# Performance work log

Hardware: AMD Instinct MI355X
Metric: run time of the kernel (lower is better)

## Reference

```python
import jax, jax.numpy as jnp
import numpy as np

HIDDEN = 3072
HEADS = 32
HEAD_DIM = HIDDEN // HEADS  # 96


def setup_inputs() -> dict:
    key = jax.random.key(0)
    k1, k2, k3, k4 = jax.random.split(key, 4)
    B, S = 2, 2048
    x = jax.random.normal(k1, (B, S, HIDDEN), dtype=jnp.float32)
    # qkv_proj: Linear(hidden, 3*hidden, bias=False); torch weight is [out,in]
    w_qkv = jax.random.normal(k2, (3 * HIDDEN, HIDDEN), dtype=jnp.float32) * (HIDDEN ** -0.5)
    # o_proj: Linear(hidden, hidden) with bias
    w_o = jax.random.normal(k3, (HIDDEN, HIDDEN), dtype=jnp.float32) * (HIDDEN ** -0.5)
    b_o = jax.random.normal(k4, (HIDDEN,), dtype=jnp.float32) * 0.01
    return {"x": x, "w_qkv": w_qkv, "w_o": w_o, "b_o": b_o}


def reference(x, w_qkv, w_o, b_o):
    B, S, _ = x.shape
    qkv = jnp.einsum('bsh,oh->bso', x, w_qkv)  # [B,S,3*HIDDEN]
    q, k, v = jnp.split(qkv, 3, axis=-1)
    # [B,S,HIDDEN] -> [B,H,S,D]
    def split_heads(t):
        return t.reshape(B, S, HEADS, HEAD_DIM).transpose(0, 2, 1, 3)
    q, k, v = split_heads(q), split_heads(k), split_heads(v)
    scores = jnp.einsum('bhqd,bhkd->bhqk', q, k) / jnp.sqrt(jnp.float32(HEAD_DIM))
    attn = jax.nn.softmax(scores, axis=-1)
    out = jnp.einsum('bhqk,bhkd->bhqd', attn, v)  # [B,H,S,D]
    out = out.transpose(0, 2, 1, 3).reshape(B, S, HIDDEN)
    return jnp.einsum('bsh,oh->bso', out, w_o) + b_o
```

## Files before the change

### kernel.cpp

```cpp
#include <hip/hip_runtime.h>
#include <math.h>


typedef unsigned int u32;
typedef unsigned short u16;
typedef __attribute__((ext_vector_type(8))) short bf16x8;
typedef __attribute__((ext_vector_type(4))) float f32x4;
typedef __attribute__((ext_vector_type(16))) float f32x16;

#define MFMA(a, b, c) __builtin_amdgcn_mfma_f32_16x16x32_bf16((a), (b), (c), 0, 0, 0)
#define MFMA32(a, b, c) __builtin_amdgcn_mfma_f32_32x32x16_bf16((a), (b), (c), 0, 0, 0)

#define GLDS16(g, l) __builtin_amdgcn_global_load_lds( \
    (const __attribute__((address_space(1))) u32*)(g), \
    (__attribute__((address_space(3))) u32*)(l), 16, 0, 0)

__device__ __forceinline__ u16 f2bf(float f) {
  u32 u = __builtin_bit_cast(u32, f);
  return (u16)((u + 0x7fffu + ((u >> 16) & 1u)) >> 16);
}
__device__ __forceinline__ float bf2f(u16 h) {
  u32 u = ((u32)h) << 16;
  return __builtin_bit_cast(float, u);
}
__device__ __forceinline__ void split2(float f, u16& h, u16& l) {
  h = f2bf(f);
  l = f2bf(f - bf2f(h));
}
__device__ __forceinline__ bf16x8 ld16(const u16* p) {
  return *reinterpret_cast<const bf16x8*>(p);
}

__global__ void split_kernel(const float* __restrict__ src, u16* __restrict__ dst,
                             long n) {
  long i = ((long)blockIdx.x * 256 + threadIdx.x) * 4;
  if (i >= n) return;
  const float4 v = *reinterpret_cast<const float4*>(src + i);
  const u32 i32 = (u32)i;
  const u32 row = i32 / 3072u;
  const u32 col = i32 - row * 3072u;
  const long base = (long)row * 6144 + (col >> 5) * 64 + (col & 31);
  ushort4 h, l;
  split2(v.x, h.x, l.x);
  split2(v.y, h.y, l.y);
  split2(v.z, h.z, l.z);
  split2(v.w, h.w, l.w);
  *reinterpret_cast<ushort4*>(dst + base) = h;
  *reinterpret_cast<ushort4*>(dst + base + 32) = l;
}

template <int MODE>
__global__ __launch_bounds__(256, 2) void gemm32(
    const u16* __restrict__ A2, const u16* __restrict__ B2,
    int M, int N,
    u16* __restrict__ C2, float* __restrict__ Cf, const float* __restrict__ bias) {
  constexpr int NT = 96;
  __shared__ u16 ldsA[2][128 * 64];
  __shared__ u16 ldsB[2][192 * 64];
  const int tid = threadIdx.x;
  const int lane = tid & 63;
  const int w = tid >> 6;
  const int wm = w >> 1, wn = w & 1;
  const int l31 = lane & 31;
  const int l5 = lane >> 5;

  const int mt = M >> 7;
  const int nwg = gridDim.x;
  const int bid = blockIdx.x;
  const int wg = (bid & 7) * (nwg >> 3) + (bid >> 3);
  const int bm = wg % mt, bn = wg / mt;

  const int srow = lane >> 3;
  const int sgc = ((lane & 7) ^ srow ^ w) * 8;

  auto stA = [&](int buf, int kt, int j) {
    const int r = j * 32 + w * 8 + srow;
    GLDS16(A2 + (long)(bm * 128 + r) * 6144 + kt * 64 + sgc,
           &ldsA[buf][(j * 32 + w * 8) * 64]);
  };
  auto stB = [&](int buf, int kt, int j) {
    const int r = j * 32 + w * 8 + srow;
    GLDS16(B2 + (long)(bn * 192 + r) * 6144 + kt * 64 + sgc,
           &ldsB[buf][(j * 32 + w * 8) * 64]);
  };

  f32x16 acc[2][3];
#pragma unroll
  for (int m = 0; m < 2; ++m)
#pragma unroll
    for (int n = 0; n < 3; ++n)
#pragma unroll
      for (int j = 0; j < 16; ++j) acc[m][n][j] = 0.f;

  stA(0, 0, 0); stA(0, 0, 1); stA(0, 0, 2); stA(0, 0, 3);
  stB(0, 0, 0); stB(0, 0, 1); stB(0, 0, 2);
  stB(0, 0, 3); stB(0, 0, 4); stB(0, 0, 5);
  __syncthreads();

  const int aRow0 = wm * 64 + l31;
  const int bRow0 = wn * 96 + l31;
  const int rk = (lane & 7) ^ ((lane >> 3) & 3);

#define CSLOT(KS, PL) ((((KS)*2 + l5 + (PL)*4) ^ rk) * 8)
#define RD_PH(KS)                                                          \
  _Pragma("unroll") for (int n = 0; n < 3; ++n) {                          \
    const int off = (bRow0 + n * 32) * 64;                                 \
    b[n][0] = ld16(&LB[off + CSLOT(KS, 0)]);                               \
    b[n][1] = ld16(&LB[off + CSLOT(KS, 1)]);                               \
  }                                                                        \
  _Pragma("unroll") for (int m = 0; m < 2; ++m) {                          \
    const int off = (aRow0 + m * 32) * 64;                                 \
    a[m][0] = ld16(&LA[off + CSLOT(KS, 0)]);                               \
    a[m][1] = ld16(&LA[off + CSLOT(KS, 1)]);                               \
  }
#define DO_MFMA3()                                                         \
  __builtin_amdgcn_s_setprio(1);                                           \
  _Pragma("unroll") for (int m = 0; m < 2; ++m)                            \
  _Pragma("unroll") for (int n = 0; n < 3; ++n) {                          \
    acc[m][n] = MFMA32(a[m][0], b[n][0], acc[m][n]);                       \
    acc[m][n] = MFMA32(a[m][0], b[n][1], acc[m][n]);                       \
    acc[m][n] = MFMA32(a[m][1], b[n][0], acc[m][n]);                       \
  }                                                                        \
  __builtin_amdgcn_s_setprio(0);
#define PH_SYNC()                                                          \
  __builtin_amdgcn_s_barrier();                                            \
  asm volatile("s_waitcnt lgkmcnt(0)" ::: "memory");                       \
  __builtin_amdgcn_sched_barrier(0);

  for (int t = 0; t < NT; ++t) {
    const int cur = t & 1;
    const int nxt = cur ^ 1;
    const u16* LA = ldsA[cur];
    const u16* LB = ldsB[cur];
    bf16x8 a[2][2], b[3][2];
    RD_PH(0);
    if (t + 1 < NT) {
      stA(nxt, t + 1, 0); stA(nxt, t + 1, 1);
      stA(nxt, t + 1, 2); stA(nxt, t + 1, 3);
      stB(nxt, t + 1, 0); stB(nxt, t + 1, 1); stB(nxt, t + 1, 2);
      stB(nxt, t + 1, 3); stB(nxt, t + 1, 4); stB(nxt, t + 1, 5);
    }
    PH_SYNC();
    DO_MFMA3();
    __builtin_amdgcn_s_barrier();
    RD_PH(1);
    PH_SYNC();
    DO_MFMA3();
    asm volatile("s_waitcnt vmcnt(0)" ::: "memory");
    __builtin_amdgcn_s_barrier();
  }
#undef CSLOT
#undef RD_PH
#undef DO_MFMA3
#undef PH_SYNC

#pragma unroll
  for (int mf = 0; mf < 2; ++mf)
#pragma unroll
    for (int nf = 0; nf < 3; ++nf) {
      const int col = bn * 192 + wn * 96 + nf * 32 + l31;
#pragma unroll
      for (int reg = 0; reg < 16; ++reg) {
        const int rif = (reg & 3) + 8 * (reg >> 2) + 4 * l5;
        const long row = (long)bm * 128 + wm * 64 + mf * 32 + rif;
        const float v = acc[mf][nf][reg];
        if (MODE == 0) {
          const long idx = row * (2L * N) + (col >> 5) * 64 + (col & 31);
          u16 h, l;
          split2(v, h, l);
          C2[idx] = h;
          C2[idx + 32] = l;
        } else {
          Cf[row * N + col] = v + bias[col];
        }
      }
    }
}

__global__ void pack_k(const u16* __restrict__ QKV2, u16* __restrict__ Kp) {
  const int t = blockIdx.x * 256 + threadIdx.x;
  const int lane = t & 63;
  const int rec3 = t >> 6;
  const int c = rec3 % 3;
  const int kb = (rec3 / 3) & 127;
  const int hl = rec3 / 384;
  const int lr = lane & 15, lg = lane >> 4;
  const long src = ((long)((hl >> 5) * 2048 + kb * 16 + lr)) * 18432 +
                   (96 + (hl & 31) * 3 + c) * 64 + lg * 8;
  const long dst = ((long)rec3 * 2) * 512 + lane * 8;
  *reinterpret_cast<bf16x8*>(Kp + dst) = ld16(QKV2 + src);
  *reinterpret_cast<bf16x8*>(Kp + dst + 512) = ld16(QKV2 + src + 32);
}

__global__ __launch_bounds__(256) void pack_v(const u16* __restrict__ QKV2,
                                              u16* __restrict__ Vp) {
  __shared__ u16 sV[2][32 * 96];
  const int tid = threadIdx.x;
  const int hl = blockIdx.x >> 6;
  const int kq = blockIdx.x & 63;
  const long rowbase = ((long)((hl >> 5) * 2048 + kq * 32)) * 18432 +
                       (192 + (hl & 31) * 3) * 64;
#pragma unroll
  for (int i = 0; i < 3; ++i) {
    const int idx = i * 256 + tid;
    const int pl = idx / 384;
    const int r2 = idx % 384;
    const int row = r2 / 12, cu = r2 % 12;
    const long src = rowbase + (long)row * 18432 + (cu >> 2) * 64 + (cu & 3) * 8 + pl * 32;
    *reinterpret_cast<bf16x8*>(&sV[pl][row * 96 + cu * 8]) = ld16(QKV2 + src);
  }
  __syncthreads();
#pragma unroll
  for (int i = 0; i < 3; ++i) {
    const int idx = i * 256 + tid;
    const int lane = idx & 63;
    const int rl = idx >> 6;
    const int n = rl >> 1, pl = rl & 1;
    const int lr = lane & 15, lg = lane >> 4;
    bf16x8 o;
#pragma unroll
    for (int e = 0; e < 8; ++e) o[e] = (short)sV[pl][(lg * 8 + e) * 96 + n * 16 + lr];
    const long dst = ((((long)hl * 6 + n) * 64 + kq) * 2 + pl) * 512 + lane * 8;
    *reinterpret_cast<bf16x8*>(Vp + dst) = o;
  }
}

__global__ __launch_bounds__(256, 2) void attn_kernel(
    const u16* __restrict__ QKV2,
    const u16* __restrict__ Kp, const u16* __restrict__ Vp,
    u16* __restrict__ AO2) {
  __shared__ u16 kv[2][24 * 512];
  __shared__ u16 pb[4][2][512];
  const int lane = threadIdx.x & 63;
  const int wv = threadIdx.x >> 6;
  const int lr = lane & 15, lg = lane >> 4;

  const int nwg = gridDim.x;
  const int bid = blockIdx.x;
  const int wg = (bid & 7) * (nwg >> 3) + (bid >> 3);
  const int hl = wg >> 5;
  const int qblk = wg & 31;
  const int b = hl >> 5;
  const int q0 = qblk * 64 + wv * 16;

  bf16x8 qh[3], ql[3];
  {
    const long qofs =
        ((long)(b * 2048 + q0 + lr)) * 18432 + ((hl & 31) * 3) * 64 + lg * 8;
#pragma unroll
    for (int c = 0; c < 3; ++c) {
      qh[c] = ld16(QKV2 + qofs + c * 64);
      ql[c] = ld16(QKV2 + qofs + c * 64 + 32);
    }
  }

  f32x4 o_acc[6];
#pragma unroll
  for (int n = 0; n < 6; ++n)
#pragma unroll
    for (int j = 0; j < 4; ++j) o_acc[n][j] = 0.f;
  float lsum[4] = {0.f, 0.f, 0.f, 0.f};

  const float scale = 0.10206207261596577f;
  u16* pbh = pb[wv][0];
  u16* pbl = pb[wv][1];

  auto stage = [&](int nb, int it) {
    const long kbase = ((long)hl * 768 + (long)it * 12) * 512;
    const long vbase = ((long)hl * 768 + (long)it * 2) * 512;
#pragma unroll
    for (int j = 0; j < 6; ++j) {
      const int r = wv * 6 + j;
      const u16* src;
      if (r < 12) {
        const int tt = r / 6, rc = r % 6;
        src = Kp + kbase + ((long)(tt * 6 + rc)) * 512 + lane * 8;
      } else {
        const int r2 = r - 12;
        src = Vp + vbase + ((long)((r2 >> 1) * 128 + (r2 & 1))) * 512 + lane * 8;
      }
      GLDS16(src, &kv[nb][r * 512]);
    }
  };

  stage(0, 0);
  __syncthreads();

  for (int it = 0; it < 64; ++it) {
    const int nb = it & 1;
    if (it < 63) stage(nb ^ 1, it + 1);
    const u16* L = kv[nb];

    f32x4 s0, s1;
#pragma unroll
    for (int j = 0; j < 4; ++j) { s0[j] = 0.f; s1[j] = 0.f; }
#pragma unroll
    for (int c = 0; c < 3; ++c) {
      const bf16x8 kh0 = ld16(L + (c * 2 + 0) * 512 + lane * 8);
      const bf16x8 kl0 = ld16(L + (c * 2 + 1) * 512 + lane * 8);
      const bf16x8 kh1 = ld16(L + (6 + c * 2 + 0) * 512 + lane * 8);
      const bf16x8 kl1 = ld16(L + (6 + c * 2 + 1) * 512 + lane * 8);
      s0 = MFMA(qh[c], kh0, s0);
      s1 = MFMA(qh[c], kh1, s1);
      s0 = MFMA(qh[c], kl0, s0);
      s1 = MFMA(qh[c], kl1, s1);
      s0 = MFMA(ql[c], kh0, s0);
      s1 = MFMA(ql[c], kh1, s1);
    }

#pragma unroll
    for (int j = 0; j < 4; ++j) {
      const float p0 = __expf(fmaf(s0[j], scale, -12.f));
      const float p1 = __expf(fmaf(s1[j], scale, -12.f));
      lsum[j] += p0 + p1;
      const int r = lg * 4 + j;
      const int key = j ^ lg;
      u16 h, l;
      split2(p0, h, l);
      const int a0 = r * 32 + ((((lr >> 3) ^ key) & 3) << 3) + (lr & 7);
      pbh[a0] = h;
      pbl[a0] = l;
      split2(p1, h, l);
      const int a1 = r * 32 + ((((2 + (lr >> 3)) ^ key) & 3) << 3) + (lr & 7);
      pbh[a1] = h;
      pbl[a1] = l;
    }
    const int rkey = (lr & 3) ^ (lr >> 2);
    const int ra = lr * 32 + (((lg ^ rkey) & 3) << 3);
    const bf16x8 pah = ld16(&pbh[ra]);
    const bf16x8 pal = ld16(&pbl[ra]);

#pragma unroll
    for (int n = 0; n < 6; ++n) {
      const bf16x8 vh = ld16(L + (12 + n * 2 + 0) * 512 + lane * 8);
      const bf16x8 vl = ld16(L + (12 + n * 2 + 1) * 512 + lane * 8);
      o_acc[n] = MFMA(pah, vh, o_acc[n]);
      o_acc[n] = MFMA(pah, vl, o_acc[n]);
      o_acc[n] = MFMA(pal, vh, o_acc[n]);
    }
    __syncthreads();
  }

  float inv[4];
#pragma unroll
  for (int j = 0; j < 4; ++j) {
    float rs = lsum[j];
#pragma unroll
    for (int mk = 1; mk < 16; mk <<= 1) rs += __shfl_xor(rs, mk);
    inv[j] = 1.f / rs;
  }
#pragma unroll
  for (int n = 0; n < 6; ++n)
#pragma unroll
    for (int j = 0; j < 4; ++j) {
      const long row = (long)(b * 2048 + q0 + lg * 4 + j);
      const long idx =
          row * 6144 + ((hl & 31) * 3 + (n >> 1)) * 64 + (n & 1) * 16 + lr;
      u16 h, l;
      split2(o_acc[n][j] * inv[j], h, l);
      AO2[idx] = h;
      AO2[idx + 32] = l;
    }
}

extern "C" void kernel_launch(void* const* d_in, const int* in_sizes, int n_in,
                              void* d_out, int out_size, void* d_ws, size_t ws_size,
                              hipStream_t stream) {
  const float* x = (const float*)d_in[0];
  const float* wqkv = (const float*)d_in[1];
  const float* wo = (const float*)d_in[2];
  const float* bo = (const float*)d_in[3];
  float* out = (float*)d_out;
  char* ws = (char*)d_ws;

  const size_t E_X = (size_t)4096 * 3072;
  const size_t E_WQ = (size_t)9216 * 3072;
  const size_t E_QKV = (size_t)4096 * 9216;
  const size_t E_WO = (size_t)3072 * 3072;

  u16* X2 = (u16*)ws;
  char* W0 = ws + 4 * E_X;
  u16* W2 = (u16*)W0;
  char* Q0 = W0 + 4 * E_WQ;
  u16* QKV2 = (u16*)Q0;
  char* V0 = Q0 + 4 * E_QKV;
  u16* VP = (u16*)V0;
  u16* KP = (u16*)ws;
  u16* AO2 = (u16*)W0;
  u16* WO2 = (u16*)(W0 + 4 * E_X);

  const size_t need = 4 * (E_X + E_WQ + E_QKV + E_X);
  if (ws_size < need) return;

  split_kernel<<<12288, 256, 0, stream>>>(x, X2, (long)E_X);
  split_kernel<<<27648, 256, 0, stream>>>(wqkv, W2, (long)E_WQ);
  gemm32<0><<<1536, 256, 0, stream>>>(X2, W2, 4096, 9216, QKV2, nullptr, nullptr);
  pack_k<<<6144, 256, 0, stream>>>(QKV2, KP);
  pack_v<<<4096, 256, 0, stream>>>(QKV2, VP);
  split_kernel<<<9216, 256, 0, stream>>>(wo, WO2, (long)E_WO);
  attn_kernel<<<2048, 256, 0, stream>>>(QKV2, KP, VP, AO2);
  gemm32<1><<<512, 256, 0, stream>>>(AO2, WO2, 4096, 3072, nullptr, out, bo);
}
```

Baseline: 1.318 ms.

## Process two 16-row query fragments per wave to reuse staged K/V tiles

Each wave now handles 32 query rows (two fragments) instead of 16, so each workgroup covers 128 queries and the grid is halved. The K and V values loaded from LDS, and the K/V tiles staged from global memory, are reused across both fragments, cutting LDS reads and global K/V traffic per query. In exchange, registers roughly double for accumulators and Q fragments, which may hurt occupancy under the two-blocks-per-CU launch bound. The grid of 1024 workgroups is also coarser across the CUs.

```diff
diff --git a/kernel.cpp b/kernel.cpp
--- a/kernel.cpp
+++ b/kernel.cpp
@@ -230,7 +230,7 @@
     const u16* __restrict__ Kp, const u16* __restrict__ Vp,
     u16* __restrict__ AO2) {
   __shared__ u16 kv[2][24 * 512];
-  __shared__ u16 pb[4][2][512];
+  __shared__ u16 pb[4][2][2][512];
   const int lane = threadIdx.x & 63;
   const int wv = threadIdx.x >> 6;
   const int lr = lane & 15, lg = lane >> 4;
@@ -238,32 +238,33 @@
   const int nwg = gridDim.x;
   const int bid = blockIdx.x;
   const int wg = (bid & 7) * (nwg >> 3) + (bid >> 3);
-  const int hl = wg >> 5;
-  const int qblk = wg & 31;
+  const int hl = wg >> 4;
+  const int qblk = wg & 15;
   const int b = hl >> 5;
-  const int q0 = qblk * 64 + wv * 16;
-
-  bf16x8 qh[3], ql[3];
-  {
+  const int q0 = qblk * 128 + wv * 32;
+
+  bf16x8 qh[2][3], ql[2][3];
+#pragma unroll
+  for (int f = 0; f < 2; ++f) {
     const long qofs =
-        ((long)(b * 2048 + q0 + lr)) * 18432 + ((hl & 31) * 3) * 64 + lg * 8;
+        ((long)(b * 2048 + q0 + f * 16 + lr)) * 18432 + ((hl & 31) * 3) * 64 + lg * 8;
 #pragma unroll
     for (int c = 0; c < 3; ++c) {
-      qh[c] = ld16(QKV2 + qofs + c * 64);
-      ql[c] = ld16(QKV2 + qofs + c * 64 + 32);
-    }
-  }
-
-  f32x4 o_acc[6];
-#pragma unroll
-  for (int n = 0; n < 6; ++n)
-#pragma unroll
-    for (int j = 0; j < 4; ++j) o_acc[n][j] = 0.f;
-  float lsum[4] = {0.f, 0.f, 0.f, 0.f};
+      qh[f][c] = ld16(QKV2 + qofs + c * 64);
+      ql[f][c] = ld16(QKV2 + qofs + c * 64 + 32);
+    }
+  }
+
+  f32x4 o_acc[2][6];
+#pragma unroll
+  for (int f = 0; f < 2; ++f)
+#pragma unroll
+    for (int n = 0; n < 6; ++n)
+#pragma unroll
+      for (int j = 0; j < 4; ++j) o_acc[f][n][j] = 0.f;
+  float lsum[2][4] = {{0.f, 0.f, 0.f, 0.f}, {0.f, 0.f, 0.f, 0.f}};
 
   const float scale = 0.10206207261596577f;
-  u16* pbh = pb[wv][0];
-  u16* pbl = pb[wv][1];
 
   auto stage = [&](int nb, int it) {
     const long kbase = ((long)hl * 768 + (long)it * 12) * 512;
@@ -291,76 +292,92 @@
     if (it < 63) stage(nb ^ 1, it + 1);
     const u16* L = kv[nb];
 
-    f32x4 s0, s1;
-#pragma unroll
-    for (int j = 0; j < 4; ++j) { s0[j] = 0.f; s1[j] = 0.f; }
+    bf16x8 kh0[3], kl0[3], kh1[3], kl1[3];
 #pragma unroll
     for (int c = 0; c < 3; ++c) {
-      const bf16x8 kh0 = ld16(L + (c * 2 + 0) * 512 + lane * 8);
-      const bf16x8 kl0 = ld16(L + (c * 2 + 1) * 512 + lane * 8);
-      const bf16x8 kh1 = ld16(L + (6 + c * 2 + 0) * 512 + lane * 8);
-      const bf16x8 kl1 = ld16(L + (6 + c * 2 + 1) * 512 + lane * 8);
-      s0 = MFMA(qh[c], kh0, s0);
-      s1 = MFMA(qh[c], kh1, s1);
-      s0 = MFMA(qh[c], kl0, s0);
-      s1 = MFMA(qh[c], kl1, s1);
-      s0 = MFMA(ql[c], kh0, s0);
-      s1 = MFMA(ql[c], kh1, s1);
-    }
-
-#pragma unroll
-    for (int j = 0; j < 4; ++j) {
-      const float p0 = __expf(fmaf(s0[j], scale, -12.f));
-      const float p1 = __expf(fmaf(s1[j], scale, -12.f));
-      lsum[j] += p0 + p1;
-      const int r = lg * 4 + j;
-      const int key = j ^ lg;
-      u16 h, l;
-      split2(p0, h, l);
-      const int a0 = r * 32 + ((((lr >> 3) ^ key) & 3) << 3) + (lr & 7);
-      pbh[a0] = h;
-      pbl[a0] = l;
-      split2(p1, h, l);
-      const int a1 = r * 32 + ((((2 + (lr >> 3)) ^ key) & 3) << 3) + (lr & 7);
-      pbh[a1] = h;
-      pbl[a1] = l;
-    }
-    const int rkey = (lr & 3) ^ (lr >> 2);
-    const int ra = lr * 32 + (((lg ^ rkey) & 3) << 3);
-    const bf16x8 pah = ld16(&pbh[ra]);
-    const bf16x8 pal = ld16(&pbl[ra]);
+      kh0[c] = ld16(L + (c * 2 + 0) * 512 + lane * 8);
+      kl0[c] = ld16(L + (c * 2 + 1) * 512 + lane * 8);
+      kh1[c] = ld16(L + (6 + c * 2 + 0) * 512 + lane * 8);
+      kl1[c] = ld16(L + (6 + c * 2 + 1) * 512 + lane * 8);
+    }
+
+    bf16x8 pah[2], pal[2];
+#pragma unroll
+    for (int f = 0; f < 2; ++f) {
+      f32x4 s0, s1;
+#pragma unroll
+      for (int j = 0; j < 4; ++j) { s0[j] = 0.f; s1[j] = 0.f; }
+#pragma unroll
+      for (int c = 0; c < 3; ++c) {
+        s0 = MFMA(qh[f][c], kh0[c], s0);
+        s1 = MFMA(qh[f][c], kh1[c], s1);
+        s0 = MFMA(qh[f][c], kl0[c], s0);
+        s1 = MFMA(qh[f][c], kl1[c], s1);
+        s0 = MFMA(ql[f][c], kh0[c], s0);
+        s1 = MFMA(ql[f][c], kh1[c], s1);
+      }
+      u16* pbh = pb[wv][f][0];
+      u16* pbl = pb[wv][f][1];
+#pragma unroll
+      for (int j = 0; j < 4; ++j) {
+        const float p0 = __expf(fmaf(s0[j], scale, -12.f));
+        const float p1 = __expf(fmaf(s1[j], scale, -12.f));
+        lsum[f][j] += p0 + p1;
+        const int r = lg * 4 + j;
+        const int key = j ^ lg;
+        u16 h, l;
+        split2(p0, h, l);
+        const int a0 = r * 32 + ((((lr >> 3) ^ key) & 3) << 3) + (lr & 7);
+        pbh[a0] = h;
+        pbl[a0] = l;
+        split2(p1, h, l);
+        const int a1 = r * 32 + ((((2 + (lr >> 3)) ^ key) & 3) << 3) + (lr & 7);
+        pbh[a1] = h;
+        pbl[a1] = l;
+      }
+      const int rkey = (lr & 3) ^ (lr >> 2);
+      const int ra = lr * 32 + (((lg ^ rkey) & 3) << 3);
+      pah[f] = ld16(&pbh[ra]);
+      pal[f] = ld16(&pbl[ra]);
+    }
 
 #pragma unroll
     for (int n = 0; n < 6; ++n) {
       const bf16x8 vh = ld16(L + (12 + n * 2 + 0) * 512 + lane * 8);
       const bf16x8 vl = ld16(L + (12 + n * 2 + 1) * 512 + lane * 8);
-      o_acc[n] = MFMA(pah, vh, o_acc[n]);
-      o_acc[n] = MFMA(pah, vl, o_acc[n]);
-      o_acc[n] = MFMA(pal, vh, o_acc[n]);
+#pragma unroll
+      for (int f = 0; f < 2; ++f) {
+        o_acc[f][n] = MFMA(pah[f], vh, o_acc[f][n]);
+        o_acc[f][n] = MFMA(pah[f], vl, o_acc[f][n]);
+        o_acc[f][n] = MFMA(pal[f], vh, o_acc[f][n]);
+      }
     }
     __syncthreads();
   }
 
-  float inv[4];
-#pragma unroll
-  for (int j = 0; j < 4; ++j) {
-    float rs = lsum[j];
-#pragma unroll
-    for (int mk = 1; mk < 16; mk <<= 1) rs += __shfl_xor(rs, mk);
-    inv[j] = 1.f / rs;
-  }
-#pragma unroll
-  for (int n = 0; n < 6; ++n)
+#pragma unroll
+  for (int f = 0; f < 2; ++f) {
+    float inv[4];
 #pragma unroll
     for (int j = 0; j < 4; ++j) {
-      const long row = (long)(b * 2048 + q0 + lg * 4 + j);
-      const long idx =
-          row * 6144 + ((hl & 31) * 3 + (n >> 1)) * 64 + (n & 1) * 16 + lr;
-      u16 h, l;
-      split2(o_acc[n][j] * inv[j], h, l);
-      AO2[idx] = h;
-      AO2[idx + 32] = l;
-    }
+      float rs = lsum[f][j];
+#pragma unroll
+      for (int mk = 1; mk < 16; mk <<= 1) rs += __shfl_xor(rs, mk);
+      inv[j] = 1.f / rs;
+    }
+#pragma unroll
+    for (int n = 0; n < 6; ++n)
+#pragma unroll
+      for (int j = 0; j < 4; ++j) {
+        const long row = (long)(b * 2048 + q0 + f * 16 + lg * 4 + j);
+        const long idx =
+            row * 6144 + ((hl & 31) * 3 + (n >> 1)) * 64 + (n & 1) * 16 + lr;
+        u16 h, l;
+        split2(o_acc[f][n][j] * inv[j], h, l);
+        AO2[idx] = h;
+        AO2[idx + 32] = l;
+      }
+  }
 }
 
 extern "C" void kernel_launch(void* const* d_in, const int* in_sizes, int n_in,
@@ -398,6 +415,6 @@
   pack_k<<<6144, 256, 0, stream>>>(QKV2, KP);
   pack_v<<<4096, 256, 0, stream>>>(QKV2, VP);
   split_kernel<<<9216, 256, 0, stream>>>(wo, WO2, (long)E_WO);
-  attn_kernel<<<2048, 256, 0, stream>>>(QKV2, KP, VP, AO2);
+  attn_kernel<<<1024, 256, 0, stream>>>(QKV2, KP, VP, AO2);
   gemm32<1><<<512, 256, 0, stream>>>(AO2, WO2, 4096, 3072, nullptr, out, bo);
 }
```

Result: faster. 1.216 ms (-7.7%).
